# Optimization experiments

Hardware: AMD Instinct MI355X
Metric: run time of the kernel (lower is better)

## Reference

```python
import jax, jax.numpy as jnp
import numpy as np

B, T, D, H, MLP_DIM = 4, 1024, 768, 12, 3072


def setup_inputs() -> dict:
    key = jax.random.key(0)
    ks = jax.random.split(key, 16)
    s = 0.02
    def n(i, shape):
        return jax.random.normal(ks[i], shape, jnp.float32) * s
    inp = {
        "x": jax.random.normal(ks[0], (B, T, D), jnp.float32),
        "y": jax.random.normal(ks[1], (B, T, D), jnp.float32),
        # self-attention (stream a = x, stream b = y), bias-free Linears
        "w_qkv_a": n(2, (D, 3 * D)), "w_out_a": n(3, (D, D)),
        "w_qkv_b": n(4, (D, 3 * D)), "w_out_b": n(5, (D, D)),
        # cross-attention
        "cw_qkv_a": n(6, (D, 3 * D)), "cw_out_a": n(7, (D, D)),
        "cw_qkv_b": n(8, (D, 3 * D)), "cw_out_b": n(9, (D, D)),
        # MLPs (Linear with bias)
        "mlp_a_w1": n(10, (D, MLP_DIM)), "mlp_a_b1": jnp.zeros((MLP_DIM,), jnp.float32),
        "mlp_a_w2": n(11, (MLP_DIM, D)), "mlp_a_b2": jnp.zeros((D,), jnp.float32),
        "mlp_b_w1": n(12, (D, MLP_DIM)), "mlp_b_b1": jnp.zeros((MLP_DIM,), jnp.float32),
        "mlp_b_w2": n(13, (MLP_DIM, D)), "mlp_b_b2": jnp.zeros((D,), jnp.float32),
    }
    for i in range(1, 7):
        inp[f"ln{i}_g"] = jnp.ones((D,), jnp.float32)
        inp[f"ln{i}_b"] = jnp.zeros((D,), jnp.float32)
    return inp


def _ln(x, g, b, eps=1e-5):
    m = x.mean(-1, keepdims=True)
    v = x.var(-1, keepdims=True)
    return (x - m) / jnp.sqrt(v + eps) * g + b


def _split_qkv(x, w, h):
    # faithful to einops 'b t (d k h) -> k b h t d' (d outermost, h innermost)
    qkv = x @ w                      # [b, t, 3D]
    b, t, _ = qkv.shape
    d = w.shape[0] // h
    qkv = qkv.reshape(b, t, d, 3, h).transpose(3, 0, 4, 1, 2)  # [3, b, h, t, d]
    return qkv[0], qkv[1], qkv[2]


def _attend(q, k, v, dk):
    a = jax.nn.softmax(jnp.einsum('bhid,bhjd->bhij', q, k) / dk, axis=-1)
    o = jnp.einsum('bhij,bhjd->bhid', a, v)
    b, h, t, d = o.shape
    return o.transpose(0, 2, 1, 3).reshape(b, t, h * d)


def reference(x, y,
              w_qkv_a, w_out_a, w_qkv_b, w_out_b,
              cw_qkv_a, cw_out_a, cw_qkv_b, cw_out_b,
              mlp_a_w1, mlp_a_b1, mlp_a_w2, mlp_a_b2,
              mlp_b_w1, mlp_b_b1, mlp_b_w2, mlp_b_b2,
              ln1_g, ln1_b, ln2_g, ln2_b, ln3_g, ln3_b,
              ln4_g, ln4_b, ln5_g, ln5_b, ln6_g, ln6_b):
    dk = np.float32(np.sqrt(D / H))
    # --- self-attention stage (pre-LN, residual); dropout = identity (eval) ---
    _x = _ln(x, ln1_g, ln1_b)
    _y = _ln(y, ln4_g, ln4_b)
    q, k, v = _split_qkv(_x, w_qkv_a, H)
    x = x + _attend(q, k, v, dk) @ w_out_a
    q, k, v = _split_qkv(_y, w_qkv_b, H)
    y = y + _attend(q, k, v, dk) @ w_out_b
    # --- cross-attention stage ---
    _x = _ln(x, ln2_g, ln2_b)
    _y = _ln(y, ln5_g, ln5_b)
    q1, k1, v1 = _split_qkv(_x, cw_qkv_a, H)
    q2, k2, v2 = _split_qkv(_y, cw_qkv_b, H)
    x = x + _attend(q2, k1, v1, dk) @ cw_out_a   # query from y, k/v from x
    y = y + _attend(q1, k2, v2, dk) @ cw_out_b   # query from x, k/v from y
    # --- MLP stage ---
    _x = _ln(x, ln3_g, ln3_b)
    _y = _ln(y, ln6_g, ln6_b)
    x = x + (jax.nn.gelu(_x @ mlp_a_w1 + mlp_a_b1, approximate=False) @ mlp_a_w2 + mlp_a_b2)
    y = y + (jax.nn.gelu(_y @ mlp_b_w1 + mlp_b_b1, approximate=False) @ mlp_b_w2 + mlp_b_b2)
    return (x, y)
```

## Files before the change

### kernel.cpp

```cpp
#include <hip/hip_runtime.h>
#include <hip/hip_bf16.h>

using bf16 = __hip_bfloat16;
typedef __bf16 bf16x8 __attribute__((ext_vector_type(8)));
typedef float f32x4 __attribute__((ext_vector_type(4)));

#define DEV __device__ __forceinline__

DEV void gload16(const void* g, void* l) {
  __builtin_amdgcn_global_load_lds((__attribute__((address_space(1))) void*)(g),
                                   (__attribute__((address_space(3))) void*)(l), 16, 0, 0);
}

DEV void mfma16(int4 a, int4 b, f32x4& c) {
  c = __builtin_amdgcn_mfma_f32_16x16x32_bf16(
      __builtin_bit_cast(bf16x8, a), __builtin_bit_cast(bf16x8, b), c, 0, 0, 0);
}

DEV unsigned short bfb(float x) { return __builtin_bit_cast(unsigned short, __float2bfloat16(x)); }

template<bool PERM>
__global__ __launch_bounds__(256) void wconv(const float* __restrict__ s0, const float* __restrict__ s1,
                                             const float* __restrict__ s2, const float* __restrict__ s3,
                                             bf16* d0, bf16* d1, bf16* d2, bf16* d3, int K, int N) {
  const float* S[4] = {s0, s1, s2, s3};
  bf16* Dd[4] = {d0, d1, d2, d3};
  const float* __restrict__ src = S[blockIdx.z];
  bf16* __restrict__ dst = Dd[blockIdx.z];
  __shared__ float tile[32][33];
  int tx = threadIdx.x, ty = threadIdx.y;
  int n0 = blockIdx.x * 32, k0 = blockIdx.y * 32;
#pragma unroll
  for (int i = 0; i < 4; i++) tile[ty + 8 * i][tx] = src[(size_t)(k0 + ty + 8 * i) * N + n0 + tx];
  __syncthreads();
#pragma unroll
  for (int i = 0; i < 4; i++) {
    int n = n0 + ty + 8 * i;
    int np;
    if (PERM) {
      int dd = n / 36; int r = n - dd * 36; int kk = r / 12; int h = r - kk * 12;
      np = kk * 768 + h * 64 + dd;
    } else np = n;
    dst[(size_t)np * K + k0 + tx] = __float2bfloat16(tile[tx][ty + 8 * i]);
  }
}

__global__ __launch_bounds__(192) void ln2(const float* __restrict__ xa, const float* __restrict__ xb,
                                           const float* __restrict__ ga, const float* __restrict__ ba,
                                           const float* __restrict__ gb, const float* __restrict__ bb,
                                           bf16* __restrict__ out) {
  int row = blockIdx.x;
  int s = row >> 12, r = row & 4095;
  const float* __restrict__ src = s ? xb : xa;
  const float* __restrict__ gp = s ? gb : ga;
  const float* __restrict__ bp = s ? bb : ba;
  int tid = threadIdx.x;
  float4 v = ((const float4*)(src + (size_t)r * 768))[tid];
  float sum = v.x + v.y + v.z + v.w;
  float sq = v.x * v.x + v.y * v.y + v.z * v.z + v.w * v.w;
#pragma unroll
  for (int o = 32; o; o >>= 1) { sum += __shfl_down(sum, o); sq += __shfl_down(sq, o); }
  __shared__ float red[6];
  int wv = tid >> 6;
  if ((tid & 63) == 0) { red[wv] = sum; red[wv + 3] = sq; }
  __syncthreads();
  sum = red[0] + red[1] + red[2];
  sq = red[3] + red[4] + red[5];
  float mean = sum * (1.f / 768.f);
  float var = sq * (1.f / 768.f) - mean * mean;
  float rstd = rsqrtf(var + 1e-5f);
  float4 g4 = ((const float4*)gp)[tid], b4 = ((const float4*)bp)[tid];
  ushort4 u;
  u.x = bfb((v.x - mean) * rstd * g4.x + b4.x);
  u.y = bfb((v.y - mean) * rstd * g4.y + b4.y);
  u.z = bfb((v.z - mean) * rstd * g4.z + b4.z);
  u.w = bfb((v.w - mean) * rstd * g4.w + b4.w);
  *(ushort4*)&out[(size_t)row * 768 + tid * 4] = u;
}

template<int EPI>
__global__ __launch_bounds__(256) void gemm_k(const bf16* __restrict__ A0, const bf16* __restrict__ A1,
                                              const bf16* __restrict__ Bt0, const bf16* __restrict__ Bt1,
                                              void* __restrict__ C0, void* __restrict__ C1,
                                              const float* __restrict__ bias0, const float* __restrict__ bias1,
                                              const float* __restrict__ res0, const float* __restrict__ res1,
                                              int N, int K) {
  int s = blockIdx.z;
  const bf16* __restrict__ A = s ? A1 : A0;
  const bf16* __restrict__ Bt = s ? Bt1 : Bt0;
  const float* __restrict__ bias = s ? bias1 : bias0;
  const float* __restrict__ res = s ? res1 : res0;
  int m0 = blockIdx.x * 128, n0 = blockIdx.y * 128;
  int tid = threadIdx.x, lane = tid & 63, w = tid >> 6;
  int g = lane >> 4, li = lane & 15;
  int wm = w >> 1, wn = w & 1;
  __shared__ __align__(16) bf16 As[2][128 * 32];
  __shared__ __align__(16) bf16 Bs[2][128 * 32];
  f32x4 acc[4][4];
  f32x4 zz = {0.f, 0.f, 0.f, 0.f};
#pragma unroll
  for (int i = 0; i < 4; i++)
#pragma unroll
    for (int j = 0; j < 4; j++) acc[i][j] = zz;

  const bf16* Ab = A + (size_t)m0 * K;
  const bf16* Bb = Bt + (size_t)n0 * K;
  int sw = (g ^ (li & 3)) << 3;

  auto stage = [&](int buf, int k0) {
#pragma unroll
    for (int i = 0; i < 2; i++) {
      int unit = w * 64 + i * 256 + lane;
      int row = unit >> 2, up = unit & 3;
      int col = (up ^ (row & 3)) << 3;
      gload16(Ab + (size_t)row * K + k0 + col, &As[buf][w * 512 + i * 2048]);
      gload16(Bb + (size_t)row * K + k0 + col, &Bs[buf][w * 512 + i * 2048]);
    }
  };

  const int nt = K >> 5;
  stage(0, 0);
  int cur = 0;
  for (int t = 0; t < nt; ++t) {
    __syncthreads();
    if (t + 1 < nt) stage(cur ^ 1, (t + 1) << 5);
    int4 af[4], bfr[4];
#pragma unroll
    for (int mi = 0; mi < 4; mi++) af[mi] = *(const int4*)&As[cur][(wm * 64 + mi * 16 + li) * 32 + sw];
#pragma unroll
    for (int ni = 0; ni < 4; ni++) bfr[ni] = *(const int4*)&Bs[cur][(wn * 64 + ni * 16 + li) * 32 + sw];
#pragma unroll
    for (int mi = 0; mi < 4; mi++)
#pragma unroll
      for (int ni = 0; ni < 4; ni++) mfma16(af[mi], bfr[ni], acc[mi][ni]);
    cur ^= 1;
  }

  int mrow0 = m0 + wm * 64;
  int col0 = n0 + wn * 64;
  if constexpr (EPI == 0) {
    bf16* qkv = (bf16*)C0;
#pragma unroll
    for (int mi = 0; mi < 4; mi++) {
      int mr = mrow0 + mi * 16 + 4 * g;
      int b = mr >> 10, t = mr & 1023;
#pragma unroll
      for (int ni = 0; ni < 4; ni++) {
        int col = col0 + ni * 16 + li;
        int kk = col / 768; int hd = col - kk * 768; int h = hd >> 6; int dd = hd & 63;
        size_t base = ((size_t)(kk * 2 + s) * 48 + b * 12 + h) * 65536;
        f32x4 v = acc[mi][ni];
        if (kk == 2) {
          ushort4 u; u.x = bfb(v[0]); u.y = bfb(v[1]); u.z = bfb(v[2]); u.w = bfb(v[3]);
          *(ushort4*)&qkv[base + (size_t)dd * 1024 + t] = u;
        } else {
#pragma unroll
          for (int ri = 0; ri < 4; ri++)
            qkv[base + (size_t)(t + ri) * 64 + dd] = __float2bfloat16(v[ri]);
        }
      }
    }
  } else if constexpr (EPI == 1) {
    float* C = (float*)(s ? C1 : C0);
#pragma unroll
    for (int mi = 0; mi < 4; mi++) {
      int mr = mrow0 + mi * 16 + 4 * g;
#pragma unroll
      for (int ni = 0; ni < 4; ni++) {
        int col = col0 + ni * 16 + li;
        float bv = bias ? bias[col] : 0.f;
#pragma unroll
        for (int ri = 0; ri < 4; ri++)
          C[(size_t)(mr + ri) * N + col] = res[(size_t)(mr + ri) * N + col] + acc[mi][ni][ri] + bv;
      }
    }
  } else {
    bf16* C = (bf16*)(s ? C1 : C0);
#pragma unroll
    for (int mi = 0; mi < 4; mi++) {
      int mr = mrow0 + mi * 16 + 4 * g;
#pragma unroll
      for (int ni = 0; ni < 4; ni++) {
        int col = col0 + ni * 16 + li;
        float bv = bias[col];
#pragma unroll
        for (int ri = 0; ri < 4; ri++) {
          float h = acc[mi][ni][ri] + bv;
          float o = 0.5f * h * (1.f + erff(h * 0.70710678118f));
          C[(size_t)(mr + ri) * N + col] = __float2bfloat16(o);
        }
      }
    }
  }
}

__global__ __launch_bounds__(256) void attn_k(const bf16* __restrict__ qkv, bf16* __restrict__ out, int cross) {
  int f = blockIdx.x;
  int qt = (f >> 3) & 7;
  int c = ((f >> 6) << 3) | (f & 7);
  int so = (c >= 48) ? 1 : 0;
  int bh = c - so * 48;
  int qs = cross ? 1 - so : so;
  const bf16* __restrict__ qp = qkv + ((size_t)qs * 48 + bh) * 65536;
  const bf16* __restrict__ kp = qkv + ((size_t)(2 + so) * 48 + bh) * 65536;
  const bf16* __restrict__ vp = qkv + ((size_t)(4 + so) * 48 + bh) * 65536;
  int tid = threadIdx.x, lane = tid & 63, w = tid >> 6, g = lane >> 4, li = lane & 15;
  __shared__ __align__(16) bf16 Ps[4][32 * 64];
  bf16* ps = Ps[w];
  int qr0 = qt * 128 + w * 32;
  int4 qf[2][2];
#pragma unroll
  for (int mi = 0; mi < 2; mi++)
#pragma unroll
    for (int ks = 0; ks < 2; ks++)
      qf[mi][ks] = *(const int4*)(qp + (size_t)(qr0 + mi * 16 + li) * 64 + ks * 32 + 8 * g);
  f32x4 o_acc[2][4];
  float m_run[2], l_run[2];
  f32x4 zz = {0.f, 0.f, 0.f, 0.f};
#pragma unroll
  for (int mi = 0; mi < 2; mi++) {
#pragma unroll
    for (int dj = 0; dj < 4; dj++) o_acc[mi][dj] = zz;
    m_run[mi] = -1e30f; l_run[mi] = 0.f;
  }
  const float C2 = 0.18033688011112042f;
  const int xsw = (li & 7);

#pragma unroll 2
  for (int kt = 0; kt < 16; ++kt) {
    f32x4 sacc[4][2];
#pragma unroll
    for (int nj = 0; nj < 4; nj++) { sacc[nj][0] = zz; sacc[nj][1] = zz; }
#pragma unroll
    for (int nj = 0; nj < 4; nj++) {
      const bf16* krow = kp + (size_t)(kt * 64 + nj * 16 + li) * 64 + 8 * g;
      int4 kf0 = *(const int4*)(krow);
      int4 kf1 = *(const int4*)(krow + 32);
      mfma16(kf0, qf[0][0], sacc[nj][0]); mfma16(kf1, qf[0][1], sacc[nj][0]);
      mfma16(kf0, qf[1][0], sacc[nj][1]); mfma16(kf1, qf[1][1], sacc[nj][1]);
    }
#pragma unroll
    for (int mi = 0; mi < 2; mi++) {
      float mx = sacc[0][mi][0];
#pragma unroll
      for (int nj = 0; nj < 4; nj++)
#pragma unroll
        for (int ri = 0; ri < 4; ri++) mx = fmaxf(mx, sacc[nj][mi][ri]);
      mx = fmaxf(mx, __shfl_xor(mx, 16));
      mx = fmaxf(mx, __shfl_xor(mx, 32));
      float mold = m_run[mi];
      float mnew = mold;
      if (!__all(mx <= mold)) {
        mnew = fmaxf(mold, mx);
        float alpha = exp2f((mold - mnew) * C2);
        l_run[mi] *= alpha;
#pragma unroll
        for (int dj = 0; dj < 4; dj++) o_acc[mi][dj] *= alpha;
        m_run[mi] = mnew;
      }
      float rs = 0.f;
#pragma unroll
      for (int nj = 0; nj < 4; nj++) {
        float p0 = exp2f((sacc[nj][mi][0] - mnew) * C2);
        float p1 = exp2f((sacc[nj][mi][1] - mnew) * C2);
        float p2 = exp2f((sacc[nj][mi][2] - mnew) * C2);
        float p3 = exp2f((sacc[nj][mi][3] - mnew) * C2);
        rs += (p0 + p1) + (p2 + p3);
        ushort4 u; u.x = bfb(p0); u.y = bfb(p1); u.z = bfb(p2); u.w = bfb(p3);
        *(ushort4*)&ps[(mi * 16 + li) * 64 + (((2 * nj + (g >> 1)) ^ xsw) << 3) + ((g & 1) << 2)] = u;
      }
      rs += __shfl_xor(rs, 16);
      rs += __shfl_xor(rs, 32);
      l_run[mi] += rs;
    }
#pragma unroll
    for (int ks2 = 0; ks2 < 2; ks2++) {
      int4 pa0 = *(const int4*)&ps[(0 * 16 + li) * 64 + (((4 * ks2 + g) ^ xsw) << 3)];
      int4 pa1 = *(const int4*)&ps[(1 * 16 + li) * 64 + (((4 * ks2 + g) ^ xsw) << 3)];
#pragma unroll
      for (int dj = 0; dj < 4; dj++) {
        int4 vf = *(const int4*)(vp + (size_t)(dj * 16 + li) * 1024 + kt * 64 + ks2 * 32 + 8 * g);
        mfma16(vf, pa0, o_acc[0][dj]);
        mfma16(vf, pa1, o_acc[1][dj]);
      }
    }
  }
  int b = bh / 12, h = bh - (bh / 12) * 12;
#pragma unroll
  for (int mi = 0; mi < 2; mi++) {
    float inv = 1.f / l_run[mi];
    int tq = qr0 + mi * 16 + li;
    size_t rowbase = ((size_t)so * 4096 + (size_t)b * 1024 + tq) * 768;
#pragma unroll
    for (int dj = 0; dj < 4; dj++) {
      ushort4 u;
      u.x = bfb(o_acc[mi][dj][0] * inv); u.y = bfb(o_acc[mi][dj][1] * inv);
      u.z = bfb(o_acc[mi][dj][2] * inv); u.w = bfb(o_acc[mi][dj][3] * inv);
      *(ushort4*)&out[rowbase + h * 64 + dj * 16 + 4 * g] = u;
    }
  }
}

extern "C" void kernel_launch(void* const* d_in, const int* in_sizes, int n_in,
                              void* d_out, int out_size, void* d_ws, size_t ws_size,
                              hipStream_t stream) {
  const float* x_in = (const float*)d_in[0];
  const float* y_in = (const float*)d_in[1];
  const float* w_qkv_a = (const float*)d_in[2];
  const float* w_out_a = (const float*)d_in[3];
  const float* w_qkv_b = (const float*)d_in[4];
  const float* w_out_b = (const float*)d_in[5];
  const float* cw_qkv_a = (const float*)d_in[6];
  const float* cw_out_a = (const float*)d_in[7];
  const float* cw_qkv_b = (const float*)d_in[8];
  const float* cw_out_b = (const float*)d_in[9];
  const float* w1a = (const float*)d_in[10]; const float* b1a = (const float*)d_in[11];
  const float* w2a = (const float*)d_in[12]; const float* b2a = (const float*)d_in[13];
  const float* w1b = (const float*)d_in[14]; const float* b1b = (const float*)d_in[15];
  const float* w2b = (const float*)d_in[16]; const float* b2b = (const float*)d_in[17];
  const float *lng[6], *lnb[6];
  for (int i = 0; i < 6; i++) { lng[i] = (const float*)d_in[18 + 2 * i]; lnb[i] = (const float*)d_in[19 + 2 * i]; }

  char* ws = (char*)d_ws;
  bf16* WQKV = (bf16*)ws;
  bf16* WOUT = (bf16*)(ws + 14155776);
  bf16* W1 = (bf16*)(ws + 18874368);
  bf16* W2 = (bf16*)(ws + 28311552);
  bf16* XN = (bf16*)(ws + 37748736);
  bf16* QKV = (bf16*)(ws + 50331648);
  bf16* AO = (bf16*)(ws + 88080384);
  bf16* MLPH = (bf16*)(ws + 50331648);
  float* X1 = (float*)(ws + 100663296);
  float* X2 = (float*)(ws + 125829120);
  float* OUT = (float*)d_out;

  dim3 tb(32, 8);
  wconv<true><<<dim3(72, 24, 4), tb, 0, stream>>>(w_qkv_a, w_qkv_b, cw_qkv_a, cw_qkv_b,
      WQKV, WQKV + 1769472, WQKV + 2 * 1769472, WQKV + 3 * 1769472, 768, 2304);
  wconv<false><<<dim3(24, 24, 4), tb, 0, stream>>>(w_out_a, w_out_b, cw_out_a, cw_out_b,
      WOUT, WOUT + 589824, WOUT + 2 * 589824, WOUT + 3 * 589824, 768, 768);
  wconv<false><<<dim3(96, 24, 2), tb, 0, stream>>>(w1a, w1b, nullptr, nullptr,
      W1, W1 + 2359296, nullptr, nullptr, 768, 3072);
  wconv<false><<<dim3(24, 96, 2), tb, 0, stream>>>(w2a, w2b, nullptr, nullptr,
      W2, W2 + 2359296, nullptr, nullptr, 3072, 768);

  ln2<<<8192, 192, 0, stream>>>(x_in, y_in, lng[0], lnb[0], lng[3], lnb[3], XN);
  gemm_k<0><<<dim3(32, 18, 2), 256, 0, stream>>>(XN, XN + 3145728, WQKV, WQKV + 1769472,
      QKV, nullptr, nullptr, nullptr, nullptr, nullptr, 2304, 768);
  attn_k<<<dim3(768, 1, 1), 256, 0, stream>>>(QKV, AO, 0);
  gemm_k<1><<<dim3(32, 6, 2), 256, 0, stream>>>(AO, AO + 3145728, WOUT, WOUT + 589824,
      X1, X1 + 3145728, nullptr, nullptr, x_in, y_in, 768, 768);
  ln2<<<8192, 192, 0, stream>>>(X1, X1 + 3145728, lng[1], lnb[1], lng[4], lnb[4], XN);
  gemm_k<0><<<dim3(32, 18, 2), 256, 0, stream>>>(XN, XN + 3145728, WQKV + 2 * 1769472, WQKV + 3 * 1769472,
      QKV, nullptr, nullptr, nullptr, nullptr, nullptr, 2304, 768);
  attn_k<<<dim3(768, 1, 1), 256, 0, stream>>>(QKV, AO, 1);
  gemm_k<1><<<dim3(32, 6, 2), 256, 0, stream>>>(AO, AO + 3145728, WOUT + 2 * 589824, WOUT + 3 * 589824,
      X2, X2 + 3145728, nullptr, nullptr, X1, X1 + 3145728, 768, 768);
  ln2<<<8192, 192, 0, stream>>>(X2, X2 + 3145728, lng[2], lnb[2], lng[5], lnb[5], XN);
  gemm_k<2><<<dim3(32, 24, 2), 256, 0, stream>>>(XN, XN + 3145728, W1, W1 + 2359296,
      MLPH, MLPH + 12582912, b1a, b1b, nullptr, nullptr, 3072, 768);
  gemm_k<1><<<dim3(32, 6, 2), 256, 0, stream>>>(MLPH, MLPH + 12582912, W2, W2 + 2359296,
      OUT, OUT + 3145728, b2a, b2b, X2, X2 + 3145728, 768, 3072);
}
```

Before: 519.3 us.

## Stage K/V tiles in LDS with double buffering and cheapen GELU and packing

After: 476.5 us. 8.2% less time.

```diff
diff --git a/kernel.cpp b/kernel.cpp
--- a/kernel.cpp
+++ b/kernel.cpp
@@ -18,6 +18,23 @@
 }
 
 DEV unsigned short bfb(float x) { return __builtin_bit_cast(unsigned short, __float2bfloat16(x)); }
+
+DEV int cvtpk(float lo, float hi) {
+  int r;
+  asm("v_cvt_pk_bf16_f32 %0, %1, %2" : "=v"(r) : "v"(lo), "v"(hi));
+  return r;
+}
+
+DEV float gelu_f(float h) {
+  float xr = h * 0.70710678118f;
+  float ax = fabsf(xr);
+  float t = __builtin_amdgcn_rcpf(fmaf(0.3275911f, ax, 1.f));
+  float poly = fmaf(fmaf(fmaf(fmaf(1.061405429f, t, -1.453152027f), t, 1.421413741f),
+                         t, -0.284496736f), t, 0.254829592f) * t;
+  float e = __expf(-xr * xr);
+  float erfv = copysignf(1.f - poly * e, xr);
+  return 0.5f * h * (1.f + erfv);
+}
 
 template<bool PERM>
 __global__ __launch_bounds__(256) void wconv(const float* __restrict__ s0, const float* __restrict__ s1,
@@ -184,11 +201,8 @@
         int col = col0 + ni * 16 + li;
         float bv = bias[col];
 #pragma unroll
-        for (int ri = 0; ri < 4; ri++) {
-          float h = acc[mi][ni][ri] + bv;
-          float o = 0.5f * h * (1.f + erff(h * 0.70710678118f));
-          C[(size_t)(mr + ri) * N + col] = __float2bfloat16(o);
-        }
+        for (int ri = 0; ri < 4; ri++)
+          C[(size_t)(mr + ri) * N + col] = __float2bfloat16(gelu_f(acc[mi][ni][ri] + bv));
       }
     }
   }
@@ -205,6 +219,8 @@
   const bf16* __restrict__ kp = qkv + ((size_t)(2 + so) * 48 + bh) * 65536;
   const bf16* __restrict__ vp = qkv + ((size_t)(4 + so) * 48 + bh) * 65536;
   int tid = threadIdx.x, lane = tid & 63, w = tid >> 6, g = lane >> 4, li = lane & 15;
+  __shared__ __align__(16) bf16 Ks[2][64 * 64];
+  __shared__ __align__(16) bf16 Vs[2][64 * 64];
   __shared__ __align__(16) bf16 Ps[4][32 * 64];
   bf16* ps = Ps[w];
   int qr0 = qt * 128 + w * 32;
@@ -226,16 +242,31 @@
   const float C2 = 0.18033688011112042f;
   const int xsw = (li & 7);
 
+  auto stage = [&](int buf, int kt) {
+#pragma unroll
+    for (int p = 0; p < 2; p++) {
+      int l = p * 256 + w * 64 + lane;
+      int r = l >> 3, u = l & 7;
+      int su = (u ^ (r & 7)) << 3;
+      gload16(kp + (size_t)(kt * 64 + r) * 64 + su, &Ks[buf][(p * 256 + w * 64) * 8]);
+      gload16(vp + (size_t)r * 1024 + kt * 64 + su, &Vs[buf][(p * 256 + w * 64) * 8]);
+    }
+  };
+
+  stage(0, 0);
+  int cur = 0;
 #pragma unroll 2
   for (int kt = 0; kt < 16; ++kt) {
+    __syncthreads();
+    if (kt < 15) stage(cur ^ 1, kt + 1);
     f32x4 sacc[4][2];
 #pragma unroll
     for (int nj = 0; nj < 4; nj++) { sacc[nj][0] = zz; sacc[nj][1] = zz; }
 #pragma unroll
     for (int nj = 0; nj < 4; nj++) {
-      const bf16* krow = kp + (size_t)(kt * 64 + nj * 16 + li) * 64 + 8 * g;
-      int4 kf0 = *(const int4*)(krow);
-      int4 kf1 = *(const int4*)(krow + 32);
+      int trow = nj * 16 + li;
+      int4 kf0 = *(const int4*)&Ks[cur][trow * 64 + ((g ^ (trow & 7)) << 3)];
+      int4 kf1 = *(const int4*)&Ks[cur][trow * 64 + (((4 + g) ^ (trow & 7)) << 3)];
       mfma16(kf0, qf[0][0], sacc[nj][0]); mfma16(kf1, qf[0][1], sacc[nj][0]);
       mfma16(kf0, qf[1][0], sacc[nj][1]); mfma16(kf1, qf[1][1], sacc[nj][1]);
     }
@@ -266,11 +297,9 @@
         float p2 = exp2f((sacc[nj][mi][2] - mnew) * C2);
         float p3 = exp2f((sacc[nj][mi][3] - mnew) * C2);
         rs += (p0 + p1) + (p2 + p3);
-        ushort4 u; u.x = bfb(p0); u.y = bfb(p1); u.z = bfb(p2); u.w = bfb(p3);
-        *(ushort4*)&ps[(mi * 16 + li) * 64 + (((2 * nj + (g >> 1)) ^ xsw) << 3) + ((g & 1) << 2)] = u;
-      }
-      rs += __shfl_xor(rs, 16);
-      rs += __shfl_xor(rs, 32);
+        int2 u2; u2.x = cvtpk(p0, p1); u2.y = cvtpk(p2, p3);
+        *(int2*)&ps[(mi * 16 + li) * 64 + (((2 * nj + (g >> 1)) ^ xsw) << 3) + ((g & 1) << 2)] = u2;
+      }
       l_run[mi] += rs;
     }
 #pragma unroll
@@ -279,16 +308,21 @@
       int4 pa1 = *(const int4*)&ps[(1 * 16 + li) * 64 + (((4 * ks2 + g) ^ xsw) << 3)];
 #pragma unroll
       for (int dj = 0; dj < 4; dj++) {
-        int4 vf = *(const int4*)(vp + (size_t)(dj * 16 + li) * 1024 + kt * 64 + ks2 * 32 + 8 * g);
+        int drow = dj * 16 + li;
+        int4 vf = *(const int4*)&Vs[cur][drow * 64 + ((((ks2 << 2) + g) ^ (drow & 7)) << 3)];
         mfma16(vf, pa0, o_acc[0][dj]);
         mfma16(vf, pa1, o_acc[1][dj]);
       }
     }
+    cur ^= 1;
   }
   int b = bh / 12, h = bh - (bh / 12) * 12;
 #pragma unroll
   for (int mi = 0; mi < 2; mi++) {
-    float inv = 1.f / l_run[mi];
+    float lt = l_run[mi];
+    lt += __shfl_xor(lt, 16);
+    lt += __shfl_xor(lt, 32);
+    float inv = 1.f / lt;
     int tq = qr0 + mi * 16 + li;
     size_t rowbase = ((size_t)so * 4096 + (size_t)b * 1024 + tq) * 768;
 #pragma unroll
```
